# Kernel tuning notes

Measured on AMD Instinct MI355X. Metric: run time of the kernel, lower is better.

## Reference

```python
import jax, jax.numpy as jnp
import numpy as np

IN_FEATURES = 20000   # genes
OUT_FEATURES = 3000   # pathways
NNZ = 600000          # sparsity = 1 - NNZ/(IN*OUT) = 0.99
BATCH = 8192          # cells


def setup_inputs() -> dict:
    key = jax.random.key(0)
    k_w, k_b, k_x = jax.random.split(key, 3)

    # Unique, coalesced (sorted by row-major flat index) COO pattern, mimicking
    # torch_sparse.coalesce: sample with slight oversampling, dedupe, truncate.
    rng = np.random.default_rng(0)
    flat = np.unique(rng.integers(0, IN_FEATURES * OUT_FEATURES,
                                  size=NNZ + 20000, dtype=np.int64))[:NNZ]
    rows = jnp.asarray(flat // IN_FEATURES, dtype=jnp.int32)   # [nnz] in [0, OUT)
    cols = jnp.asarray(flat % IN_FEATURES, dtype=jnp.int32)    # [nnz] in [0, IN)

    stdv = 1.0 / np.sqrt(OUT_FEATURES)  # reset_parameters uses 1/sqrt(out_features)
    weights = jax.random.uniform(k_w, (NNZ,), minval=-stdv, maxval=stdv,
                                 dtype=jnp.float32)
    bias = jax.random.uniform(k_b, (OUT_FEATURES,), minval=-stdv, maxval=stdv,
                              dtype=jnp.float32)
    inputs = jax.random.normal(k_x, (BATCH, IN_FEATURES), dtype=jnp.float32)
    return {"inputs": inputs, "weights": weights, "bias": bias,
            "rows": rows, "cols": cols}


def reference(inputs, weights, bias, rows, cols):
    # y = x @ W^T + b, where W is the sparse [out, in] matrix defined by
    # (rows, cols, weights). Indices are unique (coalesced), so scatter-add
    # into a dense W reproduces torch_sparse.spmm exactly.
    out_features = bias.shape[0]
    in_features = inputs.shape[-1]
    W = jnp.zeros((out_features, in_features), dtype=inputs.dtype)
    W = W.at[rows, cols].add(weights)              # [out, in] dense view of sparse W
    return inputs @ W.T + bias                     # [batch, out]
```

## Files before the change

### kernel.cpp

```cpp
#include <hip/hip_runtime.h>
#include <stdint.h>

#define IN_F   20000
#define OUT_F  3000
#define BATCH  8192

#define CHUNK     2048
#define NCHUNKS   (BATCH / CHUNK)

__global__ __launch_bounds__(256)
void k_transpose(const float* __restrict__ x, uint16_t* __restrict__ xT,
                 int b_base) {
    __shared__ uint16_t tile[128][68];
    const int c0 = blockIdx.x * 64;
    const int b0 = b_base + blockIdx.y * 128;
    const int tid = threadIdx.x;

#pragma unroll
    for (int i = 0; i < 8; ++i) {
        int idx = tid + i * 256;
        int b = idx >> 4, cq = idx & 15;
        int cc = c0 + cq * 4;
        float4 v = make_float4(0.f, 0.f, 0.f, 0.f);
        if (cc < IN_F)
            v = *(const float4*)&x[(size_t)(b0 + b) * IN_F + cc];
        uint32_t u0 = __float_as_uint(v.x), u1 = __float_as_uint(v.y);
        uint32_t u2 = __float_as_uint(v.z), u3 = __float_as_uint(v.w);
        uint32_t r0 = (u0 + 0x7fffu + ((u0 >> 16) & 1u)) >> 16;
        uint32_t r1 = (u1 + 0x7fffu + ((u1 >> 16) & 1u)) >> 16;
        uint32_t r2 = (u2 + 0x7fffu + ((u2 >> 16) & 1u)) >> 16;
        uint32_t r3 = (u3 + 0x7fffu + ((u3 >> 16) & 1u)) >> 16;
        uint2 pk = make_uint2(r0 | (r1 << 16), r2 | (r3 << 16));
        *(uint2*)&tile[b][cq * 4] = pk;
    }
    __syncthreads();

#pragma unroll
    for (int i = 0; i < 16; ++i) {
        int idx = tid + i * 256;
        int c = idx >> 6, bp = idx & 63;
        int cc = c0 + c;
        if (cc < IN_F) {
            uint32_t lo = tile[2 * bp + 0][c];
            uint32_t hi = tile[2 * bp + 1][c];
            *(uint32_t*)&xT[(size_t)cc * BATCH + (b0 + 2 * bp)] = lo | (hi << 16);
        }
    }
}

__global__ __launch_bounds__(256)
void k_row_ptr(const int* __restrict__ rows, int* __restrict__ row_ptr, int nnz) {
    int k = blockIdx.x * 256 + threadIdx.x;
    if (k >= nnz) return;
    int r  = rows[k];
    int rp = (k == 0) ? -1 : rows[k - 1];
    for (int q = rp + 1; q <= r; ++q) row_ptr[q] = k;
    if (k == nnz - 1) {
        for (int q = r + 1; q <= OUT_F; ++q) row_ptr[q] = nnz;
    }
}

#define ROWS_PB 16
#define BT      64
#define NRG     ((OUT_F + ROWS_PB - 1) / ROWS_PB)
#define NTILES  (CHUNK / BT)
#define TPX     (NTILES / 8)

#define BF_LO(u) __uint_as_float((u) << 16)
#define BF_HI(u) __uint_as_float((u) & 0xffff0000u)
#define FMA8(A, q, wv)                                              \
    A[0] = fmaf(wv, BF_LO((q).x), A[0]);                            \
    A[1] = fmaf(wv, BF_HI((q).x), A[1]);                            \
    A[2] = fmaf(wv, BF_LO((q).y), A[2]);                            \
    A[3] = fmaf(wv, BF_HI((q).y), A[3]);                            \
    A[4] = fmaf(wv, BF_LO((q).z), A[4]);                            \
    A[5] = fmaf(wv, BF_HI((q).z), A[5]);                            \
    A[6] = fmaf(wv, BF_LO((q).w), A[6]);                            \
    A[7] = fmaf(wv, BF_HI((q).w), A[7]);

__global__ __launch_bounds__(128, 8)
void k_spmm(const uint16_t* __restrict__ xT, const float* __restrict__ w,
            const float* __restrict__ bias, const int* __restrict__ cols,
            const int* __restrict__ row_ptr, float* __restrict__ out,
            int b_base) {
    const int i = blockIdx.x;
    const int xcd = i & 7;
    const int j = i >> 3;
    const int tile_local = j / NRG;
    const int row_grp   = j - tile_local * NRG;
    const int tile = xcd + 8 * tile_local;
    const int b0 = b_base + tile * BT;

    const int t = threadIdx.x;
    const int row_sub = t >> 3;
    const int lane8  = t & 7;
    const int r = row_grp * ROWS_PB + row_sub;
    if (r >= OUT_F) return;

    const int kbeg = row_ptr[r];
    const int kend = row_ptr[r + 1];

    const uint16_t* xbase = xT + (size_t)(b0 + lane8 * 8);

    float acc[8];
#pragma unroll
    for (int e = 0; e < 8; ++e) acc[e] = 0.f;

    int k = kbeg;
    int   c0n = 0, c1n = 0, c2n = 0, c3n = 0;
    float w0n = 0.f, w1n = 0.f, w2n = 0.f, w3n = 0.f;
    if (k + 3 < kend) {
        c0n = cols[k];     c1n = cols[k + 1];
        c2n = cols[k + 2]; c3n = cols[k + 3];
        w0n = w[k];     w1n = w[k + 1];
        w2n = w[k + 2]; w3n = w[k + 3];
    }
    while (k + 3 < kend) {
        const int   c0 = c0n, c1 = c1n, c2 = c2n, c3 = c3n;
        const float w0 = w0n, w1 = w1n, w2 = w2n, w3 = w3n;
        uint4 q0 = *(const uint4*)(xbase + ((size_t)c0 << 13));
        uint4 q1 = *(const uint4*)(xbase + ((size_t)c1 << 13));
        uint4 q2 = *(const uint4*)(xbase + ((size_t)c2 << 13));
        uint4 q3 = *(const uint4*)(xbase + ((size_t)c3 << 13));
        k += 4;
        if (k + 3 < kend) {
            c0n = cols[k];     c1n = cols[k + 1];
            c2n = cols[k + 2]; c3n = cols[k + 3];
            w0n = w[k];     w1n = w[k + 1];
            w2n = w[k + 2]; w3n = w[k + 3];
        }
        FMA8(acc, q0, w0);
        FMA8(acc, q1, w1);
        FMA8(acc, q2, w2);
        FMA8(acc, q3, w3);
    }
    for (; k < kend; ++k) {
        int   c  = cols[k];
        float wv = w[k];
        uint4 q = *(const uint4*)(xbase + ((size_t)c << 13));
        FMA8(acc, q, wv);
    }

    const float bv = bias[r];
    const int   bb = b0 + lane8 * 8;
#pragma unroll
    for (int e = 0; e < 8; ++e) {
        out[(size_t)(bb + e) * OUT_F + r] = acc[e] + bv;
    }
}

extern "C" void kernel_launch(void* const* d_in, const int* in_sizes, int n_in,
                              void* d_out, int out_size, void* d_ws, size_t ws_size,
                              hipStream_t stream) {
    const float* x    = (const float*)d_in[0];
    const float* w    = (const float*)d_in[1];
    const float* bias = (const float*)d_in[2];
    const int*   rows = (const int*)d_in[3];
    const int*   cols = (const int*)d_in[4];
    float*       out  = (float*)d_out;
    const int    nnz  = in_sizes[1];

    int*      row_ptr = (int*)d_ws;
    uint16_t* xT      = (uint16_t*)((char*)d_ws + 16384);

    hipLaunchKernelGGL(k_row_ptr, dim3((nnz + 255) / 256), dim3(256), 0, stream,
                       rows, row_ptr, nnz);

    dim3 gT((IN_F + 63) / 64, CHUNK / 128);
    for (int ch = 0; ch < NCHUNKS; ++ch) {
        int b_base = ch * CHUNK;
        hipLaunchKernelGGL(k_transpose, gT, dim3(256), 0, stream, x, xT, b_base);
        hipLaunchKernelGGL(k_spmm, dim3(8 * TPX * NRG), dim3(128), 0, stream,
                           xT, w, bias, cols, row_ptr, out, b_base);
    }
}
```

Measured before the change: 2.164 ms.

## Restructure SpMM to one wave per row and stage output through shared memory

The SpMM kernel is remapped so that each 64-lane wave owns one output row and covers 512 batch columns, where before 8 lanes per row covered 64. Each block handles 4 rows, collects results in LDS and writes coalesced float4 stores instead of scalar stores strided by OUT_F. The gather loop becomes a software pipeline that prefetches the next four xT rows before doing the FMAs. The chunk size is doubled and each transpose block now loops over 8 column tiles to cut the number of blocks. Risks are less row parallelism per block, idle waves on rows with uneven nnz, and the larger xT chunk spilling out of cache.

Result: faster. 1.980 ms (-8.5%).

```diff
diff --git a/kernel.cpp b/kernel.cpp
--- a/kernel.cpp
+++ b/kernel.cpp
@@ -5,45 +5,53 @@
 #define OUT_F  3000
 #define BATCH  8192
 
-#define CHUNK     2048
+#define CHUNK     4096
 #define NCHUNKS   (BATCH / CHUNK)
 
+#define TW 8
 __global__ __launch_bounds__(256)
 void k_transpose(const float* __restrict__ x, uint16_t* __restrict__ xT,
                  int b_base) {
     __shared__ uint16_t tile[128][68];
-    const int c0 = blockIdx.x * 64;
-    const int b0 = b_base + blockIdx.y * 128;
+    const int b0  = b_base + blockIdx.y * 128;
     const int tid = threadIdx.x;
+    const int cbase = blockIdx.x * (64 * TW);
+
+    for (int s = 0; s < TW; ++s) {
+        const int c0 = cbase + s * 64;
+        if (c0 >= IN_F) break;
+        if (s) __syncthreads();
 
 #pragma unroll
-    for (int i = 0; i < 8; ++i) {
-        int idx = tid + i * 256;
-        int b = idx >> 4, cq = idx & 15;
-        int cc = c0 + cq * 4;
-        float4 v = make_float4(0.f, 0.f, 0.f, 0.f);
-        if (cc < IN_F)
-            v = *(const float4*)&x[(size_t)(b0 + b) * IN_F + cc];
-        uint32_t u0 = __float_as_uint(v.x), u1 = __float_as_uint(v.y);
-        uint32_t u2 = __float_as_uint(v.z), u3 = __float_as_uint(v.w);
-        uint32_t r0 = (u0 + 0x7fffu + ((u0 >> 16) & 1u)) >> 16;
-        uint32_t r1 = (u1 + 0x7fffu + ((u1 >> 16) & 1u)) >> 16;
-        uint32_t r2 = (u2 + 0x7fffu + ((u2 >> 16) & 1u)) >> 16;
-        uint32_t r3 = (u3 + 0x7fffu + ((u3 >> 16) & 1u)) >> 16;
-        uint2 pk = make_uint2(r0 | (r1 << 16), r2 | (r3 << 16));
-        *(uint2*)&tile[b][cq * 4] = pk;
-    }
-    __syncthreads();
+        for (int i = 0; i < 8; ++i) {
+            int idx = tid + i * 256;
+            int b = idx >> 4, cq = idx & 15;
+            int cc = c0 + cq * 4;
+            float4 v = make_float4(0.f, 0.f, 0.f, 0.f);
+            if (cc < IN_F)
+                v = *(const float4*)&x[(size_t)(b0 + b) * IN_F + cc];
+            uint32_t u0 = __float_as_uint(v.x), u1 = __float_as_uint(v.y);
+            uint32_t u2 = __float_as_uint(v.z), u3 = __float_as_uint(v.w);
+            uint32_t r0 = (u0 + 0x7fffu + ((u0 >> 16) & 1u)) >> 16;
+            uint32_t r1 = (u1 + 0x7fffu + ((u1 >> 16) & 1u)) >> 16;
+            uint32_t r2 = (u2 + 0x7fffu + ((u2 >> 16) & 1u)) >> 16;
+            uint32_t r3 = (u3 + 0x7fffu + ((u3 >> 16) & 1u)) >> 16;
+            uint2 pk = make_uint2(r0 | (r1 << 16), r2 | (r3 << 16));
+            *(uint2*)&tile[b][cq * 4] = pk;
+        }
+        __syncthreads();
 
 #pragma unroll
-    for (int i = 0; i < 16; ++i) {
-        int idx = tid + i * 256;
-        int c = idx >> 6, bp = idx & 63;
-        int cc = c0 + c;
-        if (cc < IN_F) {
-            uint32_t lo = tile[2 * bp + 0][c];
-            uint32_t hi = tile[2 * bp + 1][c];
-            *(uint32_t*)&xT[(size_t)cc * BATCH + (b0 + 2 * bp)] = lo | (hi << 16);
+        for (int i = 0; i < 16; ++i) {
+            int idx = tid + i * 256;
+            int c = idx >> 6, bp = idx & 63;
+            int cc = c0 + c;
+            if (cc < IN_F) {
+                uint32_t lo = tile[2 * bp + 0][c];
+                uint32_t hi = tile[2 * bp + 1][c];
+                *(uint32_t*)&xT[(size_t)cc * BATCH + (b0 + 2 * bp)] =
+                    lo | (hi << 16);
+            }
         }
     }
 }
@@ -60,11 +68,9 @@
     }
 }
 
-#define ROWS_PB 16
-#define BT      64
-#define NRG     ((OUT_F + ROWS_PB - 1) / ROWS_PB)
+#define BT      512
 #define NTILES  (CHUNK / BT)
-#define TPX     (NTILES / 8)
+#define NRG     (OUT_F / 4)
 
 #define BF_LO(u) __uint_as_float((u) << 16)
 #define BF_HI(u) __uint_as_float((u) & 0xffff0000u)
@@ -78,74 +84,80 @@
     A[6] = fmaf(wv, BF_LO((q).w), A[6]);                            \
     A[7] = fmaf(wv, BF_HI((q).w), A[7]);
 
-__global__ __launch_bounds__(128, 8)
+__global__ __launch_bounds__(256, 8)
 void k_spmm(const uint16_t* __restrict__ xT, const float* __restrict__ w,
             const float* __restrict__ bias, const int* __restrict__ cols,
             const int* __restrict__ row_ptr, float* __restrict__ out,
             int b_base) {
-    const int i = blockIdx.x;
-    const int xcd = i & 7;
-    const int j = i >> 3;
-    const int tile_local = j / NRG;
-    const int row_grp   = j - tile_local * NRG;
-    const int tile = xcd + 8 * tile_local;
-    const int b0 = b_base + tile * BT;
+    __shared__ float ot[4][520];
 
-    const int t = threadIdx.x;
-    const int row_sub = t >> 3;
-    const int lane8  = t & 7;
-    const int r = row_grp * ROWS_PB + row_sub;
-    if (r >= OUT_F) return;
+    const int blk  = blockIdx.x;
+    const int tile = blk & 7;
+    const int rg   = blk >> 3;
+    const int b0   = b_base + tile * BT;
+
+    const int wv = __builtin_amdgcn_readfirstlane(threadIdx.x >> 6);
+    const int l  = threadIdx.x & 63;
+    const int r  = rg * 4 + wv;
 
     const int kbeg = row_ptr[r];
     const int kend = row_ptr[r + 1];
 
-    const uint16_t* xbase = xT + (size_t)(b0 + lane8 * 8);
+    const uint16_t* xb = xT + ((size_t)b0 + l * 8);
 
     float acc[8];
 #pragma unroll
     for (int e = 0; e < 8; ++e) acc[e] = 0.f;
 
     int k = kbeg;
-    int   c0n = 0, c1n = 0, c2n = 0, c3n = 0;
-    float w0n = 0.f, w1n = 0.f, w2n = 0.f, w3n = 0.f;
-    if (k + 3 < kend) {
-        c0n = cols[k];     c1n = cols[k + 1];
-        c2n = cols[k + 2]; c3n = cols[k + 3];
-        w0n = w[k];     w1n = w[k + 1];
-        w2n = w[k + 2]; w3n = w[k + 3];
+    uint4 qa0 = make_uint4(0, 0, 0, 0), qa1 = qa0, qa2 = qa0, qa3 = qa0;
+    if (k + 4 <= kend) {
+        qa0 = *(const uint4*)(xb + ((size_t)cols[k + 0] << 13));
+        qa1 = *(const uint4*)(xb + ((size_t)cols[k + 1] << 13));
+        qa2 = *(const uint4*)(xb + ((size_t)cols[k + 2] << 13));
+        qa3 = *(const uint4*)(xb + ((size_t)cols[k + 3] << 13));
     }
-    while (k + 3 < kend) {
-        const int   c0 = c0n, c1 = c1n, c2 = c2n, c3 = c3n;
-        const float w0 = w0n, w1 = w1n, w2 = w2n, w3 = w3n;
-        uint4 q0 = *(const uint4*)(xbase + ((size_t)c0 << 13));
-        uint4 q1 = *(const uint4*)(xbase + ((size_t)c1 << 13));
-        uint4 q2 = *(const uint4*)(xbase + ((size_t)c2 << 13));
-        uint4 q3 = *(const uint4*)(xbase + ((size_t)c3 << 13));
+    while (k + 8 <= kend) {
+        float w0 = w[k + 0], w1 = w[k + 1], w2 = w[k + 2], w3 = w[k + 3];
+        uint4 qb0 = *(const uint4*)(xb + ((size_t)cols[k + 4] << 13));
+        uint4 qb1 = *(const uint4*)(xb + ((size_t)cols[k + 5] << 13));
+        uint4 qb2 = *(const uint4*)(xb + ((size_t)cols[k + 6] << 13));
+        uint4 qb3 = *(const uint4*)(xb + ((size_t)cols[k + 7] << 13));
+        FMA8(acc, qa0, w0);
+        FMA8(acc, qa1, w1);
+        FMA8(acc, qa2, w2);
+        FMA8(acc, qa3, w3);
+        qa0 = qb0; qa1 = qb1; qa2 = qb2; qa3 = qb3;
         k += 4;
-        if (k + 3 < kend) {
-            c0n = cols[k];     c1n = cols[k + 1];
-            c2n = cols[k + 2]; c3n = cols[k + 3];
-            w0n = w[k];     w1n = w[k + 1];
-            w2n = w[k + 2]; w3n = w[k + 3];
-        }
-        FMA8(acc, q0, w0);
-        FMA8(acc, q1, w1);
-        FMA8(acc, q2, w2);
-        FMA8(acc, q3, w3);
+    }
+    if (k + 4 <= kend) {
+        float w0 = w[k + 0], w1 = w[k + 1], w2 = w[k + 2], w3 = w[k + 3];
+        FMA8(acc, qa0, w0);
+        FMA8(acc, qa1, w1);
+        FMA8(acc, qa2, w2);
+        FMA8(acc, qa3, w3);
+        k += 4;
     }
     for (; k < kend; ++k) {
-        int   c  = cols[k];
-        float wv = w[k];
-        uint4 q = *(const uint4*)(xbase + ((size_t)c << 13));
-        FMA8(acc, q, wv);
+        float wvl = w[k];
+        uint4 q = *(const uint4*)(xb + ((size_t)cols[k] << 13));
+        FMA8(acc, q, wvl);
     }
 
     const float bv = bias[r];
-    const int   bb = b0 + lane8 * 8;
 #pragma unroll
-    for (int e = 0; e < 8; ++e) {
-        out[(size_t)(bb + e) * OUT_F + r] = acc[e] + bv;
+    for (int e = 0; e < 8; ++e) acc[e] += bv;
+
+    *(float4*)&ot[wv][l * 8 + 0] = make_float4(acc[0], acc[1], acc[2], acc[3]);
+    *(float4*)&ot[wv][l * 8 + 4] = make_float4(acc[4], acc[5], acc[6], acc[7]);
+    __syncthreads();
+
+    const int rb = rg * 4;
+#pragma unroll
+    for (int i = 0; i < 2; ++i) {
+        int bb = threadIdx.x + i * 256;
+        float4 o = make_float4(ot[0][bb], ot[1][bb], ot[2][bb], ot[3][bb]);
+        *(float4*)&out[(size_t)(b0 + bb) * OUT_F + rb] = o;
     }
 }
 
@@ -166,11 +178,11 @@
     hipLaunchKernelGGL(k_row_ptr, dim3((nnz + 255) / 256), dim3(256), 0, stream,
                        rows, row_ptr, nnz);
 
-    dim3 gT((IN_F + 63) / 64, CHUNK / 128);
+    dim3 gT((IN_F + 64 * TW - 1) / (64 * TW), CHUNK / 128);
     for (int ch = 0; ch < NCHUNKS; ++ch) {
         int b_base = ch * CHUNK;
         hipLaunchKernelGGL(k_transpose, gT, dim3(256), 0, stream, x, xT, b_base);
-        hipLaunchKernelGGL(k_spmm, dim3(8 * TPX * NRG), dim3(128), 0, stream,
+        hipLaunchKernelGGL(k_spmm, dim3(NTILES * NRG), dim3(256), 0, stream,
                            xT, w, bias, cols, row_ptr, out, b_base);
     }
 }
```
